# Kernel optimization log

Measured on AMD Instinct MI355X. Metric: run time of the kernel, lower is better.

The kernel has to match this reference:

```python
import jax, jax.numpy as jnp
import numpy as np

# ---- config matching init_kwargs ----
B, D, U = 8192, 1024, 512
F, E, T = 4, 4, 2
MAX_VAL = 10000000000.0
MIN_VAL = -10000000000.0
DISC_IDX = np.array([[0, 1, 2, 3], [4, 5, 6, 7]])  # discrete fields 0,1: per-expert feature index
CONT_IDX = np.array([8, 9])                         # continuous fields 2,3: single feature index
BOUNDS = np.array([-0.5, 0.0, 0.5])                 # 3 boundaries -> 4 buckets per continuous field
LOWERS = np.concatenate([[MIN_VAL], BOUNDS]).astype(np.float32)
UPPERS = np.concatenate([BOUNDS, [MAX_VAL]]).astype(np.float32)


def setup_inputs() -> dict:
    key = jax.random.key(0)
    ks = jax.random.split(key, 8)
    s_in = 1.0 / np.sqrt(D)
    s_cat = 1.0 / np.sqrt(2 * U)
    x = jax.random.normal(ks[0], (B, D), dtype=jnp.float32)
    Wc = jax.random.normal(ks[1], (D, U), dtype=jnp.float32) * s_in      # common expert kernel
    bc = jnp.zeros((U,), dtype=jnp.float32)
    We = jax.random.normal(ks[2], (F, E, D, U), dtype=jnp.float32) * s_in  # per-field per-expert kernels
    be = jnp.zeros((F, E, U), dtype=jnp.float32)
    Wg = jax.random.normal(ks[3], (T, D, F + 1), dtype=jnp.float32) * s_in  # per-task gate kernels
    bg = jnp.zeros((T, F + 1), dtype=jnp.float32)
    Wa = jax.random.normal(ks[4], (F, 2 * U, 1), dtype=jnp.float32) * s_cat  # attention kernels
    ba = jnp.zeros((F, 1), dtype=jnp.float32)
    Wu = jax.random.normal(ks[5], (F, 2 * U, 1), dtype=jnp.float32) * s_cat  # update kernels
    bu = jnp.zeros((F, 1), dtype=jnp.float32)
    return {"x": x, "Wc": Wc, "bc": bc, "We": We, "be": be,
            "Wg": Wg, "bg": bg, "Wa": Wa, "ba": ba, "Wu": Wu, "bu": bu}


def _field_masks(x):
    # discrete fields: expert j active iff x[:, idx[i][j]] > 0
    m_disc = x[:, DISC_IDX] > 0.0                         # [B, 2, E]
    # continuous fields: bucket x[:, idx] by boundaries (lower < v <= upper)
    v = x[:, CONT_IDX][..., None]                         # [B, 2, 1]
    m_cont = (v > LOWERS) & (v <= UPPERS)                 # [B, 2, E]
    return jnp.concatenate([m_disc, m_cont], axis=1).astype(x.dtype)  # [B, F, E]


def reference(x, Wc, bc, We, be, Wg, bg, Wa, ba, Wu, bu):
    # common expert: [B, U]
    common = jax.nn.relu(x @ Wc + bc)
    # all field experts at once: [B, F, E, U]
    e = jax.nn.relu(jnp.einsum('bd,fedu->bfeu', x, We) + be)
    mask = _field_masks(x)                                # [B, F, E]
    # mask-select active expert(s) per field: [B, F, U]
    field_out = jnp.einsum('bfe,bfeu->bfu', mask, e)
    # concat [common, field] per field: [B, F, 2U]
    cat = jnp.concatenate(
        [jnp.broadcast_to(common[:, None, :], field_out.shape), field_out], axis=-1)
    # sigmoid attention reweights field expert output
    att = jax.nn.sigmoid(jnp.einsum('bfk,fko->bfo', cat, Wa) + ba[None])   # [B, F, 1]
    field_att = att * field_out
    # sigmoid update gate blends field expert with common expert
    upd = jax.nn.sigmoid(jnp.einsum('bfk,fko->bfo', cat, Wu) + bu[None])   # [B, F, 1]
    field_final = upd * field_att + (1.0 - upd) * common[:, None, :]       # [B, F, U]
    # experts = [common] + per-field outputs: [B, F+1, U]
    experts = jnp.concatenate([common[:, None, :], field_final], axis=1)
    # per-task softmax gates over F+1 experts: [B, T, F+1]
    gates = jax.nn.softmax(jnp.einsum('bd,tdg->btg', x, Wg) + bg[None], axis=-1)
    # task outputs: [B, T, U]
    return jnp.einsum('btg,bgu->btu', gates, experts)
```

## Files before the change

kernel.cpp:

```cpp
#include <hip/hip_runtime.h>

typedef unsigned short ushort_t;

#define B_SZ 8192
#define D_SZ 1024
#define U_SZ 512
#define F_SZ 4
#define E_SZ 4
#define T_SZ 2

typedef __attribute__((ext_vector_type(8))) short bf16x8;
typedef __attribute__((ext_vector_type(4))) float f32x4;
typedef __attribute__((ext_vector_type(8))) unsigned short u16x8;

__device__ __forceinline__ unsigned short f2bf(float f) {
  union { float f; unsigned int u; } v; v.f = f;
  unsigned int r = v.u + 0x7FFFu + ((v.u >> 16) & 1u);
  return (unsigned short)(r >> 16);
}
__device__ __forceinline__ float bf2f(unsigned short h) {
  union { unsigned int u; float f; } v; v.u = ((unsigned int)h) << 16;
  return v.f;
}

__device__ __forceinline__ void gload_lds16(const void* g, void* l) {
  __builtin_amdgcn_global_load_lds(
      (const __attribute__((address_space(1))) unsigned int*)g,
      (__attribute__((address_space(3))) unsigned int*)l, 16, 0, 0);
}

__global__ __launch_bounds__(256) void conv_x(const float* __restrict__ x,
                                              ushort_t* __restrict__ xbf) {
  const size_t i = ((size_t)blockIdx.x * 256 + threadIdx.x) * 8;
  const float4 a = *(const float4*)(x + i);
  const float4 c = *(const float4*)(x + i + 4);
  u16x8 o;
  o[0] = f2bf(a.x); o[1] = f2bf(a.y); o[2] = f2bf(a.z); o[3] = f2bf(a.w);
  o[4] = f2bf(c.x); o[5] = f2bf(c.y); o[6] = f2bf(c.z); o[7] = f2bf(c.w);
  *(u16x8*)(xbf + i) = o;
}

__global__ __launch_bounds__(128) void pat_k(const float* __restrict__ x,
                                             unsigned int* __restrict__ pat,
                                             unsigned int* __restrict__ rowinfo,
                                             int* __restrict__ blockhist) {
  __shared__ int hist[64];
  const int t = threadIdx.x;
  if (t < 64) hist[t] = 0;
  __syncthreads();
  const int b = blockIdx.x * 128 + t;
  const float4 a = *(const float4*)(x + (size_t)b * D_SZ);
  const float4 c = *(const float4*)(x + (size_t)b * D_SZ + 4);
  const float v0 = x[(size_t)b * D_SZ + 8];
  const float v1 = x[(size_t)b * D_SZ + 9];
  int pp[4];
  pp[0] = (int)(a.x > 0.f) | ((int)(a.y > 0.f) << 1) |
          ((int)(a.z > 0.f) << 2) | ((int)(a.w > 0.f) << 3);
  pp[1] = (int)(c.x > 0.f) | ((int)(c.y > 0.f) << 1) |
          ((int)(c.z > 0.f) << 2) | ((int)(c.w > 0.f) << 3);
  const float LO[4] = {-1e10f, -0.5f, 0.f, 0.5f};
  const float HI[4] = {-0.5f, 0.f, 0.5f, 1e10f};
  pp[2] = 0; pp[3] = 0;
#pragma unroll
  for (int j = 0; j < 4; ++j) {
    if ((v0 > LO[j]) && (v0 <= HI[j])) pp[2] = 1 << j;
    if ((v1 > LO[j]) && (v1 <= HI[j])) pp[3] = 1 << j;
  }
  pat[b] = (unsigned int)(pp[0] | (pp[1] << 4) | (pp[2] << 8) | (pp[3] << 12));
  unsigned int info = 0;
#pragma unroll
  for (int f = 0; f < 4; ++f) {
    if (pp[f]) {
      const int lp = atomicAdd(&hist[f * 16 + pp[f]], 1);
      info |= (unsigned int)lp << (8 * f);
    }
  }
  rowinfo[b] = info;
  __syncthreads();
  if (t < 64) blockhist[blockIdx.x * 64 + t] = hist[t];
}

__global__ __launch_bounds__(64) void scan_k(const int* __restrict__ blockhist,
                                             int* __restrict__ base,
                                             int* __restrict__ cnt,
                                             int* __restrict__ dir,
                                             int* __restrict__ ntiles) {
  const int fp = threadIdx.x;
  int run = 0;
  for (int blk = 0; blk < 64; ++blk) {
    base[blk * 64 + fp] = run;
    run += blockhist[blk * 64 + fp];
  }
  cnt[fp] = run;
  __syncthreads();
  if (fp < 4) {
    const int f = fp;
    int idx = 0;
    for (int pop = 4; pop >= 1; --pop) {
      for (int p = 1; p < 16; ++p) {
        if (__popc(p) != pop) continue;
        const int n = cnt[f * 16 + p];
        const int nt = (n + 127) >> 7;
        for (int k = 0; k < nt; ++k) dir[f * 80 + idx++] = p | (k << 8);
      }
    }
    ntiles[f] = idx;
  }
}

__global__ __launch_bounds__(128) void scat_k(const unsigned int* __restrict__ pat,
                                              const unsigned int* __restrict__ rowinfo,
                                              const int* __restrict__ base,
                                              int* __restrict__ rowidx) {
  const int t = threadIdx.x;
  const int b = blockIdx.x * 128 + t;
  const unsigned int pv = pat[b];
  const unsigned int info = rowinfo[b];
#pragma unroll
  for (int f = 0; f < 4; ++f) {
    const int p = (int)((pv >> (4 * f)) & 15u);
    if (p) {
      const int pos = base[blockIdx.x * 64 + f * 16 + p] + (int)((info >> (8 * f)) & 255u);
      rowidx[((size_t)(f * 16 + p)) * B_SZ + pos] = b;
    }
  }
}

__global__ __launch_bounds__(256) void conv_w(const float* __restrict__ Wc,
                                              const float* __restrict__ We,
                                              ushort_t* __restrict__ wbf) {
  const int blk = blockIdx.x;
  const int midx = blk >> 7;
  const int tid = blk & 127;
  const int trow = (tid >> 3) * 64;
  const int tcol = (tid & 7) * 64;
  const float* src = (midx == 0) ? Wc : (We + (size_t)(midx - 1) * D_SZ * U_SZ);
  ushort_t* dst = wbf + (size_t)midx * U_SZ * D_SZ;

  __shared__ float tile[64][69];
  const int t = threadIdx.x;
  const int r0 = t >> 2;
  const int cseg = (t & 3) * 16;
#pragma unroll
  for (int j = 0; j < 4; ++j) {
    const float4 v = *(const float4*)(src + (size_t)(trow + r0) * U_SZ + tcol + cseg + j * 4);
    tile[r0][cseg + j * 4 + 0] = v.x;
    tile[r0][cseg + j * 4 + 1] = v.y;
    tile[r0][cseg + j * 4 + 2] = v.z;
    tile[r0][cseg + j * 4 + 3] = v.w;
  }
  __syncthreads();
  const int u = t >> 2;
  const int d0 = (t & 3) * 16;
#pragma unroll
  for (int h = 0; h < 2; ++h) {
    u16x8 ov;
#pragma unroll
    for (int k = 0; k < 8; ++k) ov[k] = f2bf(tile[d0 + h * 8 + k][u]);
    *(u16x8*)(dst + (size_t)(tcol + u) * D_SZ + trow + d0 + h * 8) = ov;
  }
}

__global__ __launch_bounds__(256) void gates_k(const float* __restrict__ x,
                                               const float* __restrict__ Wg,
                                               const float* __restrict__ bg,
                                               float* __restrict__ gates) {
  __shared__ float wgT[10 * 1024];
  const int t = threadIdx.x;
#pragma unroll
  for (int j = 0; j < 40; ++j) {
    const int i = j * 256 + t;
    const int t2 = i / 5120;
    const int rem = i - t2 * 5120;
    const int d = rem / 5;
    const int g = rem - d * 5;
    wgT[(t2 * 5 + g) * 1024 + d] = Wg[i];
  }
  __syncthreads();
  const int lane = t & 63;
  const int w = t >> 6;
#pragma unroll
  for (int rr = 0; rr < 2; ++rr) {
    const int b = blockIdx.x * 8 + w * 2 + rr;
    const float* xr = x + (size_t)b * D_SZ;
    float p[10];
#pragma unroll
    for (int j = 0; j < 10; ++j) p[j] = 0.f;
#pragma unroll
    for (int i = 0; i < 4; ++i) {
      const int d0 = i * 256 + lane * 4;
      const float4 xv = *(const float4*)(xr + d0);
#pragma unroll
      for (int g = 0; g < 10; ++g) {
        const float4 wv = *(const float4*)(wgT + g * 1024 + d0);
        p[g] += xv.x * wv.x + xv.y * wv.y + xv.z * wv.z + xv.w * wv.w;
      }
    }
#pragma unroll
    for (int off = 32; off > 0; off >>= 1)
#pragma unroll
      for (int j = 0; j < 10; ++j) p[j] += __shfl_xor(p[j], off);
    float l[10];
#pragma unroll
    for (int j = 0; j < 10; ++j) l[j] = p[j] + bg[j];
    const float mx0 = fmaxf(fmaxf(fmaxf(l[0], l[1]), fmaxf(l[2], l[3])), l[4]);
    const float mx1 = fmaxf(fmaxf(fmaxf(l[5], l[6]), fmaxf(l[7], l[8])), l[9]);
    float ev[10]; float s0 = 0.f, s1 = 0.f;
#pragma unroll
    for (int g = 0; g < 5; ++g) { ev[g] = expf(l[g] - mx0); s0 += ev[g]; }
#pragma unroll
    for (int g = 5; g < 10; ++g) { ev[g] = expf(l[g] - mx1); s1 += ev[g]; }
    if (lane < 5) gates[(size_t)b * 10 + lane] = ev[lane] / s0;
    else if (lane < 10) gates[(size_t)b * 10 + lane] = ev[lane] / s1;
  }
}

__global__ __launch_bounds__(256, 2) void gemm2(
    const ushort_t* __restrict__ xbf, const ushort_t* __restrict__ wbf,
    const int* __restrict__ rowidx, const int* __restrict__ cnt,
    const int* __restrict__ dir, const int* __restrict__ ntiles,
    const float* __restrict__ bc, const float* __restrict__ be,
    ushort_t* __restrict__ common, ushort_t* __restrict__ fout) {
  __shared__ ushort_t Ash[128 * 64];
  __shared__ ushort_t Bsh[128 * 64];
  __shared__ int ridx[128];

  const int t = threadIdx.x;
  const int lane = t & 63;
  const int w = t >> 6;
  const int wm = w >> 1;
  const int wn = w & 1;
  const int quad = lane >> 4;
  const int l16 = lane & 15;
  const int f = blockIdx.y;
  const int slot = blockIdx.x;
  const int u0 = blockIdx.z * 128;
  const bool isCommon = (f == 4);

  int p = 0, nrows = 128;
  if (isCommon) {
    if (slot >= 64) return;
    if (t < 128) ridx[t] = slot * 128 + t;
  } else {
    if (slot >= ntiles[f]) return;
    const int entry = dir[f * 80 + slot];
    p = entry & 15;
    const int tw = entry >> 8;
    const int n = cnt[f * 16 + p];
    const int rbase = tw * 128;
    nrows = min(128, n - rbase);
    if (t < 128) {
      const int rr = rbase + ((t < nrows) ? t : 0);
      ridx[t] = rowidx[((size_t)f * 16 + p) * B_SZ + rr];
    }
  }
  __syncthreads();

  size_t aoff[4]; int boff[4]; int ldsoff[4];
#pragma unroll
  for (int i = 0; i < 4; ++i) {
    const int c = (w * 4 + i) * 64 + lane;
    const int r = c >> 3;
    const int gc = (c & 7) ^ (r & 7);
    aoff[i] = (size_t)ridx[r] * D_SZ + gc * 8;
    boff[i] = r * D_SZ + gc * 8;
    ldsoff[i] = (w * 4 + i) * 1024;
  }

  int rowA[4], rowB[4];
#pragma unroll
  for (int i = 0; i < 4; ++i) {
    rowA[i] = wm * 64 + i * 16 + l16;
    rowB[i] = wn * 64 + i * 16 + l16;
  }
  int sw[2];
  sw[0] = ((quad) ^ (l16 & 7)) * 8;
  sw[1] = ((4 + quad) ^ (l16 & 7)) * 8;

  int elist[4]; int ne = 0;
  if (isCommon) { elist[0] = 0; ne = 1; }
  else {
#pragma unroll
    for (int e = 0; e < 4; ++e)
      if (p & (1 << e)) elist[ne++] = e;
  }

  const f32x4 fzero = {0.f, 0.f, 0.f, 0.f};
  f32x4 facc[4][4];
#pragma unroll
  for (int mi = 0; mi < 4; ++mi)
#pragma unroll
    for (int ni = 0; ni < 4; ++ni) facc[mi][ni] = fzero;

  for (int ei = 0; ei < ne; ++ei) {
    const int midx = isCommon ? 0 : (1 + f * 4 + elist[ei]);
    const ushort_t* wbase = wbf + (size_t)midx * (U_SZ * D_SZ) + (size_t)u0 * D_SZ;
    f32x4 acc[4][4];
#pragma unroll
    for (int mi = 0; mi < 4; ++mi)
#pragma unroll
      for (int ni = 0; ni < 4; ++ni) acc[mi][ni] = fzero;

    for (int k0 = 0; k0 < D_SZ; k0 += 64) {
#pragma unroll
      for (int i = 0; i < 4; ++i) {
        gload_lds16(xbf + aoff[i] + k0, (char*)Ash + ldsoff[i]);
        gload_lds16(wbase + boff[i] + k0, (char*)Bsh + ldsoff[i]);
      }
      __syncthreads();
#pragma unroll
      for (int qs = 0; qs < 2; ++qs) {
        bf16x8 av[4], bv[4];
#pragma unroll
        for (int mi = 0; mi < 4; ++mi)
          av[mi] = *(const bf16x8*)(Ash + rowA[mi] * 64 + sw[qs]);
#pragma unroll
        for (int ni = 0; ni < 4; ++ni)
          bv[ni] = *(const bf16x8*)(Bsh + rowB[ni] * 64 + sw[qs]);
#pragma unroll
        for (int mi = 0; mi < 4; ++mi)
#pragma unroll
          for (int ni = 0; ni < 4; ++ni)
            acc[mi][ni] = __builtin_amdgcn_mfma_f32_16x16x32_bf16(av[mi], bv[ni],
                                                                  acc[mi][ni], 0, 0, 0);
      }
      __syncthreads();
    }

    if (isCommon) {
#pragma unroll
      for (int mi = 0; mi < 4; ++mi) {
        const int rowb = slot * 128 + wm * 64 + mi * 16 + quad * 4;
#pragma unroll
        for (int ni = 0; ni < 4; ++ni) {
          const int u = u0 + wn * 64 + ni * 16 + l16;
          const float bcv = bc[u];
#pragma unroll
          for (int r = 0; r < 4; ++r) {
            const float v = fmaxf(acc[mi][ni][r] + bcv, 0.f);
            common[(size_t)(rowb + r) * U_SZ + u] = f2bf(v);
          }
        }
      }
    } else {
      const float* bevp = be + (size_t)(f * 4 + elist[ei]) * U_SZ;
#pragma unroll
      for (int ni = 0; ni < 4; ++ni) {
        const int u = u0 + wn * 64 + ni * 16 + l16;
        const float bev = bevp[u];
#pragma unroll
        for (int mi = 0; mi < 4; ++mi)
#pragma unroll
          for (int r = 0; r < 4; ++r)
            facc[mi][ni][r] += fmaxf(acc[mi][ni][r] + bev, 0.f);
      }
    }
  }

  if (!isCommon) {
#pragma unroll
    for (int mi = 0; mi < 4; ++mi) {
      const int rowl = wm * 64 + mi * 16 + quad * 4;
#pragma unroll
      for (int r = 0; r < 4; ++r) {
        if (rowl + r < nrows) {
          const int brow = ridx[rowl + r];
#pragma unroll
          for (int ni = 0; ni < 4; ++ni) {
            const int u = u0 + wn * 64 + ni * 16 + l16;
            fout[((size_t)brow * F_SZ + f) * U_SZ + u] = f2bf(facc[mi][ni][r]);
          }
        }
      }
    }
  }
}

__global__ __launch_bounds__(256) void stage2_k(
    const ushort_t* __restrict__ common, const ushort_t* __restrict__ fout,
    const unsigned int* __restrict__ pat, const float* __restrict__ gates,
    const float* __restrict__ Wa, const float* __restrict__ ba,
    const float* __restrict__ Wu, const float* __restrict__ bu,
    float* __restrict__ out) {
  const int b = blockIdx.x;
  const int t = threadIdx.x;
  const int lane = t & 63;
  const int w = t >> 6;
  const unsigned int pv = pat[b];

  const float c0 = bf2f(common[(size_t)b * U_SZ + t]);
  const float c1 = bf2f(common[(size_t)b * U_SZ + 256 + t]);
  float fo0[4], fo1[4];
#pragma unroll
  for (int f = 0; f < 4; ++f) {
    const bool act = ((pv >> (4 * f)) & 15u) != 0u;
    fo0[f] = act ? bf2f(fout[((size_t)b * F_SZ + f) * U_SZ + t]) : 0.f;
    fo1[f] = act ? bf2f(fout[((size_t)b * F_SZ + f) * U_SZ + 256 + t]) : 0.f;
  }
  float pa[4], pu[4];
#pragma unroll
  for (int f = 0; f < 4; ++f) {
    const float* wa = Wa + f * 1024;
    pa[f] = c0 * wa[t] + c1 * wa[256 + t] + fo0[f] * wa[512 + t] + fo1[f] * wa[768 + t];
    const float* wu = Wu + f * 1024;
    pu[f] = c0 * wu[t] + c1 * wu[256 + t] + fo0[f] * wu[512 + t] + fo1[f] * wu[768 + t];
  }
#pragma unroll
  for (int off = 32; off > 0; off >>= 1) {
#pragma unroll
    for (int f = 0; f < 4; ++f) {
      pa[f] += __shfl_xor(pa[f], off);
      pu[f] += __shfl_xor(pu[f], off);
    }
  }
  __shared__ float redA[4][4];
  __shared__ float redU[4][4];
  __shared__ float gsh[10];
  if (lane == 0) {
#pragma unroll
    for (int f = 0; f < 4; ++f) { redA[w][f] = pa[f]; redU[w][f] = pu[f]; }
  }
  if (t < 10) gsh[t] = gates[(size_t)b * 10 + t];
  __syncthreads();
  float ff0[4], ff1[4];
#pragma unroll
  for (int f = 0; f < 4; ++f) {
    const float sa = redA[0][f] + redA[1][f] + redA[2][f] + redA[3][f] + ba[f];
    const float su = redU[0][f] + redU[1][f] + redU[2][f] + redU[3][f] + bu[f];
    const float att = 1.f / (1.f + expf(-sa));
    const float upd = 1.f / (1.f + expf(-su));
    ff0[f] = upd * (att * fo0[f]) + (1.f - upd) * c0;
    ff1[f] = upd * (att * fo1[f]) + (1.f - upd) * c1;
  }
#pragma unroll
  for (int t2 = 0; t2 < 2; ++t2) {
    float v0 = gsh[t2 * 5] * c0;
    float v1 = gsh[t2 * 5] * c1;
#pragma unroll
    for (int f = 0; f < 4; ++f) {
      v0 += gsh[t2 * 5 + 1 + f] * ff0[f];
      v1 += gsh[t2 * 5 + 1 + f] * ff1[f];
    }
    out[((size_t)b * T_SZ + t2) * U_SZ + t] = v0;
    out[((size_t)b * T_SZ + t2) * U_SZ + 256 + t] = v1;
  }
}

extern "C" void kernel_launch(void* const* d_in, const int* in_sizes, int n_in,
                              void* d_out, int out_size, void* d_ws, size_t ws_size,
                              hipStream_t stream) {
  (void)in_sizes; (void)n_in; (void)out_size; (void)ws_size;
  const float* x  = (const float*)d_in[0];
  const float* Wc = (const float*)d_in[1];
  const float* bc = (const float*)d_in[2];
  const float* We = (const float*)d_in[3];
  const float* be = (const float*)d_in[4];
  const float* Wg = (const float*)d_in[5];
  const float* bg = (const float*)d_in[6];
  const float* Wa = (const float*)d_in[7];
  const float* ba = (const float*)d_in[8];
  const float* Wu = (const float*)d_in[9];
  const float* bu = (const float*)d_in[10];
  float* out = (float*)d_out;
  char* ws = (char*)d_ws;

  const size_t O_XBF    = 0;
  const size_t O_WBF    = O_XBF + (size_t)B_SZ * D_SZ * 2;
  const size_t O_PAT    = O_WBF + (size_t)17 * U_SZ * D_SZ * 2;
  const size_t O_ROWIDX = O_PAT + (size_t)B_SZ * 4;
  const size_t O_CNT    = O_ROWIDX + (size_t)4 * 16 * B_SZ * 4;
  const size_t O_DIR    = O_CNT + 256;
  const size_t O_NT     = O_DIR + 1280;
  const size_t O_GATES  = O_NT + 16;
  const size_t O_COMMON = O_GATES + (size_t)B_SZ * 10 * 4;
  const size_t O_FOUT   = O_COMMON + (size_t)B_SZ * U_SZ * 2;
  const size_t O_RINFO  = O_FOUT + (size_t)B_SZ * F_SZ * U_SZ * 2;
  const size_t O_BHIST  = O_RINFO + (size_t)B_SZ * 4;
  const size_t O_BASE   = O_BHIST + 64 * 64 * 4;

  ushort_t* xbf     = (ushort_t*)(ws + O_XBF);
  ushort_t* wbf     = (ushort_t*)(ws + O_WBF);
  unsigned int* patp= (unsigned int*)(ws + O_PAT);
  int*      rowidxp = (int*)(ws + O_ROWIDX);
  int*      cntp    = (int*)(ws + O_CNT);
  int*      dirp    = (int*)(ws + O_DIR);
  int*      ntp     = (int*)(ws + O_NT);
  float*    gatesp  = (float*)(ws + O_GATES);
  ushort_t* commonp = (ushort_t*)(ws + O_COMMON);
  ushort_t* foutp   = (ushort_t*)(ws + O_FOUT);
  unsigned int* rinfop = (unsigned int*)(ws + O_RINFO);
  int*      bhistp  = (int*)(ws + O_BHIST);
  int*      basep   = (int*)(ws + O_BASE);

  conv_x<<<dim3(4096), dim3(256), 0, stream>>>(x, xbf);
  pat_k<<<dim3(64), dim3(128), 0, stream>>>(x, patp, rinfop, bhistp);
  scan_k<<<dim3(1), dim3(64), 0, stream>>>(bhistp, basep, cntp, dirp, ntp);
  scat_k<<<dim3(64), dim3(128), 0, stream>>>(patp, rinfop, basep, rowidxp);
  conv_w<<<dim3(17 * 128), dim3(256), 0, stream>>>(Wc, We, wbf);
  gates_k<<<dim3(1024), dim3(256), 0, stream>>>(x, Wg, bg, gatesp);
  gemm2<<<dim3(80, 5, 4), dim3(256), 0, stream>>>(xbf, wbf, rowidxp, cntp, dirp, ntp,
                                                  bc, be, commonp, foutp);
  stage2_k<<<dim3(8192), dim3(256), 0, stream>>>(commonp, foutp, patp, gatesp,
                                                 Wa, ba, Wu, bu, out);
}
```

Before: 331.3 us.

## Merge prep kernels into one launch and widen GEMM tile to 256 columns

Folds the x conversion, weight transpose-conversion, gate softmax and pattern histogram kernels into a single prep kernel dispatched by block index, and merges scan and scatter into one 1024-thread block. This cuts launch count and the small serial kernels between stages. The grouped GEMM now uses 512-thread blocks covering 256 output columns, so each A tile loaded from gathered rows is reused across twice as many columns, at the cost of more LDS per block. The scan/scatter stage now runs in one block, which serialises that work.

```diff
diff --git a/kernel.cpp b/kernel.cpp
--- a/kernel.cpp
+++ b/kernel.cpp
@@ -29,212 +29,208 @@
       (__attribute__((address_space(3))) unsigned int*)l, 16, 0, 0);
 }
 
-__global__ __launch_bounds__(256) void conv_x(const float* __restrict__ x,
-                                              ushort_t* __restrict__ xbf) {
-  const size_t i = ((size_t)blockIdx.x * 256 + threadIdx.x) * 8;
-  const float4 a = *(const float4*)(x + i);
-  const float4 c = *(const float4*)(x + i + 4);
-  u16x8 o;
-  o[0] = f2bf(a.x); o[1] = f2bf(a.y); o[2] = f2bf(a.z); o[3] = f2bf(a.w);
-  o[4] = f2bf(c.x); o[5] = f2bf(c.y); o[6] = f2bf(c.z); o[7] = f2bf(c.w);
-  *(u16x8*)(xbf + i) = o;
-}
-
-__global__ __launch_bounds__(128) void pat_k(const float* __restrict__ x,
-                                             unsigned int* __restrict__ pat,
-                                             unsigned int* __restrict__ rowinfo,
-                                             int* __restrict__ blockhist) {
-  __shared__ int hist[64];
+__global__ __launch_bounds__(256) void prep_k(
+    const float* __restrict__ x, const float* __restrict__ Wc,
+    const float* __restrict__ We, const float* __restrict__ Wg,
+    const float* __restrict__ bg,
+    ushort_t* __restrict__ xbf, ushort_t* __restrict__ wbf,
+    float* __restrict__ gates, unsigned int* __restrict__ pat,
+    unsigned int* __restrict__ rowinfo, int* __restrict__ blockhist) {
+  __shared__ __align__(16) char smem[40960];
+  const int bid = blockIdx.x;
   const int t = threadIdx.x;
-  if (t < 64) hist[t] = 0;
+
+  if (bid < 4096) {
+    const size_t i = ((size_t)bid * 256 + t) * 8;
+    const float4 a = *(const float4*)(x + i);
+    const float4 c = *(const float4*)(x + i + 4);
+    u16x8 o;
+    o[0] = f2bf(a.x); o[1] = f2bf(a.y); o[2] = f2bf(a.z); o[3] = f2bf(a.w);
+    o[4] = f2bf(c.x); o[5] = f2bf(c.y); o[6] = f2bf(c.z); o[7] = f2bf(c.w);
+    *(u16x8*)(xbf + i) = o;
+  } else if (bid < 6272) {
+    const int blk = bid - 4096;
+    const int midx = blk >> 7;
+    const int tid = blk & 127;
+    const int trow = (tid >> 3) * 64;
+    const int tcol = (tid & 7) * 64;
+    const float* src = (midx == 0) ? Wc : (We + (size_t)(midx - 1) * D_SZ * U_SZ);
+    ushort_t* dst = wbf + (size_t)midx * U_SZ * D_SZ;
+    float (*tile)[69] = (float(*)[69])smem;
+    const int r0 = t >> 2;
+    const int cseg = (t & 3) * 16;
+#pragma unroll
+    for (int j = 0; j < 4; ++j) {
+      const float4 v = *(const float4*)(src + (size_t)(trow + r0) * U_SZ + tcol + cseg + j * 4);
+      tile[r0][cseg + j * 4 + 0] = v.x;
+      tile[r0][cseg + j * 4 + 1] = v.y;
+      tile[r0][cseg + j * 4 + 2] = v.z;
+      tile[r0][cseg + j * 4 + 3] = v.w;
+    }
+    __syncthreads();
+    const int u = t >> 2;
+    const int d0 = (t & 3) * 16;
+#pragma unroll
+    for (int h = 0; h < 2; ++h) {
+      u16x8 ov;
+#pragma unroll
+      for (int k = 0; k < 8; ++k) ov[k] = f2bf(tile[d0 + h * 8 + k][u]);
+      *(u16x8*)(dst + (size_t)(tcol + u) * D_SZ + trow + d0 + h * 8) = ov;
+    }
+  } else if (bid < 7296) {
+    const int gb = bid - 6272;
+    float* wgT = (float*)smem;
+#pragma unroll
+    for (int j = 0; j < 40; ++j) {
+      const int i = j * 256 + t;
+      const int t2 = i / 5120;
+      const int rem = i - t2 * 5120;
+      const int d = rem / 5;
+      const int g = rem - d * 5;
+      wgT[(t2 * 5 + g) * 1024 + d] = Wg[i];
+    }
+    __syncthreads();
+    const int lane = t & 63;
+    const int w = t >> 6;
+#pragma unroll
+    for (int rr = 0; rr < 2; ++rr) {
+      const int b = gb * 8 + w * 2 + rr;
+      const float* xr = x + (size_t)b * D_SZ;
+      float p[10];
+#pragma unroll
+      for (int j = 0; j < 10; ++j) p[j] = 0.f;
+#pragma unroll
+      for (int i = 0; i < 4; ++i) {
+        const int d0 = i * 256 + lane * 4;
+        const float4 xv = *(const float4*)(xr + d0);
+#pragma unroll
+        for (int g = 0; g < 10; ++g) {
+          const float4 wv = *(const float4*)(wgT + g * 1024 + d0);
+          p[g] += xv.x * wv.x + xv.y * wv.y + xv.z * wv.z + xv.w * wv.w;
+        }
+      }
+#pragma unroll
+      for (int off = 32; off > 0; off >>= 1)
+#pragma unroll
+        for (int j = 0; j < 10; ++j) p[j] += __shfl_xor(p[j], off);
+      float l[10];
+#pragma unroll
+      for (int j = 0; j < 10; ++j) l[j] = p[j] + bg[j];
+      const float mx0 = fmaxf(fmaxf(fmaxf(l[0], l[1]), fmaxf(l[2], l[3])), l[4]);
+      const float mx1 = fmaxf(fmaxf(fmaxf(l[5], l[6]), fmaxf(l[7], l[8])), l[9]);
+      float ev[10]; float s0 = 0.f, s1 = 0.f;
+#pragma unroll
+      for (int g = 0; g < 5; ++g) { ev[g] = expf(l[g] - mx0); s0 += ev[g]; }
+#pragma unroll
+      for (int g = 5; g < 10; ++g) { ev[g] = expf(l[g] - mx1); s1 += ev[g]; }
+      if (lane < 5) gates[(size_t)b * 10 + lane] = ev[lane] / s0;
+      else if (lane < 10) gates[(size_t)b * 10 + lane] = ev[lane] / s1;
+    }
+  } else {
+    const int pb = bid - 7296;
+    int* hist = (int*)smem;
+    if (t < 64) hist[t] = 0;
+    __syncthreads();
+    const int b = pb * 256 + t;
+    const float4 a = *(const float4*)(x + (size_t)b * D_SZ);
+    const float4 c = *(const float4*)(x + (size_t)b * D_SZ + 4);
+    const float v0 = x[(size_t)b * D_SZ + 8];
+    const float v1 = x[(size_t)b * D_SZ + 9];
+    int pp[4];
+    pp[0] = (int)(a.x > 0.f) | ((int)(a.y > 0.f) << 1) |
+            ((int)(a.z > 0.f) << 2) | ((int)(a.w > 0.f) << 3);
+    pp[1] = (int)(c.x > 0.f) | ((int)(c.y > 0.f) << 1) |
+            ((int)(c.z > 0.f) << 2) | ((int)(c.w > 0.f) << 3);
+    const float LO[4] = {-1e10f, -0.5f, 0.f, 0.5f};
+    const float HI[4] = {-0.5f, 0.f, 0.5f, 1e10f};
+    pp[2] = 0; pp[3] = 0;
+#pragma unroll
+    for (int j = 0; j < 4; ++j) {
+      if ((v0 > LO[j]) && (v0 <= HI[j])) pp[2] = 1 << j;
+      if ((v1 > LO[j]) && (v1 <= HI[j])) pp[3] = 1 << j;
+    }
+    pat[b] = (unsigned int)(pp[0] | (pp[1] << 4) | (pp[2] << 8) | (pp[3] << 12));
+    unsigned int info = 0;
+#pragma unroll
+    for (int f = 0; f < 4; ++f) {
+      if (pp[f]) {
+        const int lp = atomicAdd(&hist[f * 16 + pp[f]], 1);
+        info |= (unsigned int)lp << (8 * f);
+      }
+    }
+    rowinfo[b] = info;
+    __syncthreads();
+    if (t < 64) blockhist[pb * 64 + t] = hist[t];
+  }
+}
+
+__global__ __launch_bounds__(1024) void scanscat_k(
+    const int* __restrict__ blockhist, const unsigned int* __restrict__ pat,
+    const unsigned int* __restrict__ rowinfo,
+    int* __restrict__ rowidx, int* __restrict__ cnt,
+    int* __restrict__ dir, int* __restrict__ ntiles) {
+  __shared__ int sbase[32 * 64];
+  const int t = threadIdx.x;
+  if (t < 64) {
+    int run = 0;
+    for (int blk = 0; blk < 32; ++blk) {
+      sbase[blk * 64 + t] = run;
+      run += blockhist[blk * 64 + t];
+    }
+    cnt[t] = run;
+  }
   __syncthreads();
-  const int b = blockIdx.x * 128 + t;
-  const float4 a = *(const float4*)(x + (size_t)b * D_SZ);
-  const float4 c = *(const float4*)(x + (size_t)b * D_SZ + 4);
-  const float v0 = x[(size_t)b * D_SZ + 8];
-  const float v1 = x[(size_t)b * D_SZ + 9];
-  int pp[4];
-  pp[0] = (int)(a.x > 0.f) | ((int)(a.y > 0.f) << 1) |
-          ((int)(a.z > 0.f) << 2) | ((int)(a.w > 0.f) << 3);
-  pp[1] = (int)(c.x > 0.f) | ((int)(c.y > 0.f) << 1) |
-          ((int)(c.z > 0.f) << 2) | ((int)(c.w > 0.f) << 3);
-  const float LO[4] = {-1e10f, -0.5f, 0.f, 0.5f};
-  const float HI[4] = {-0.5f, 0.f, 0.5f, 1e10f};
-  pp[2] = 0; pp[3] = 0;
-#pragma unroll
-  for (int j = 0; j < 4; ++j) {
-    if ((v0 > LO[j]) && (v0 <= HI[j])) pp[2] = 1 << j;
-    if ((v1 > LO[j]) && (v1 <= HI[j])) pp[3] = 1 << j;
-  }
-  pat[b] = (unsigned int)(pp[0] | (pp[1] << 4) | (pp[2] << 8) | (pp[3] << 12));
-  unsigned int info = 0;
-#pragma unroll
-  for (int f = 0; f < 4; ++f) {
-    if (pp[f]) {
-      const int lp = atomicAdd(&hist[f * 16 + pp[f]], 1);
-      info |= (unsigned int)lp << (8 * f);
-    }
-  }
-  rowinfo[b] = info;
-  __syncthreads();
-  if (t < 64) blockhist[blockIdx.x * 64 + t] = hist[t];
-}
-
-__global__ __launch_bounds__(64) void scan_k(const int* __restrict__ blockhist,
-                                             int* __restrict__ base,
-                                             int* __restrict__ cnt,
-                                             int* __restrict__ dir,
-                                             int* __restrict__ ntiles) {
-  const int fp = threadIdx.x;
-  int run = 0;
-  for (int blk = 0; blk < 64; ++blk) {
-    base[blk * 64 + fp] = run;
-    run += blockhist[blk * 64 + fp];
-  }
-  cnt[fp] = run;
-  __syncthreads();
-  if (fp < 4) {
-    const int f = fp;
+  if (t < 4) {
+    const int f = t;
     int idx = 0;
     for (int pop = 4; pop >= 1; --pop) {
       for (int p = 1; p < 16; ++p) {
         if (__popc(p) != pop) continue;
-        const int n = cnt[f * 16 + p];
+        int n = 0;
+        for (int blk = 0; blk < 32; ++blk) n += blockhist[blk * 64 + f * 16 + p];
         const int nt = (n + 127) >> 7;
         for (int k = 0; k < nt; ++k) dir[f * 80 + idx++] = p | (k << 8);
       }
     }
     ntiles[f] = idx;
   }
-}
-
-__global__ __launch_bounds__(128) void scat_k(const unsigned int* __restrict__ pat,
-                                              const unsigned int* __restrict__ rowinfo,
-                                              const int* __restrict__ base,
-                                              int* __restrict__ rowidx) {
-  const int t = threadIdx.x;
-  const int b = blockIdx.x * 128 + t;
-  const unsigned int pv = pat[b];
-  const unsigned int info = rowinfo[b];
-#pragma unroll
-  for (int f = 0; f < 4; ++f) {
-    const int p = (int)((pv >> (4 * f)) & 15u);
-    if (p) {
-      const int pos = base[blockIdx.x * 64 + f * 16 + p] + (int)((info >> (8 * f)) & 255u);
-      rowidx[((size_t)(f * 16 + p)) * B_SZ + pos] = b;
-    }
-  }
-}
-
-__global__ __launch_bounds__(256) void conv_w(const float* __restrict__ Wc,
-                                              const float* __restrict__ We,
-                                              ushort_t* __restrict__ wbf) {
-  const int blk = blockIdx.x;
-  const int midx = blk >> 7;
-  const int tid = blk & 127;
-  const int trow = (tid >> 3) * 64;
-  const int tcol = (tid & 7) * 64;
-  const float* src = (midx == 0) ? Wc : (We + (size_t)(midx - 1) * D_SZ * U_SZ);
-  ushort_t* dst = wbf + (size_t)midx * U_SZ * D_SZ;
-
-  __shared__ float tile[64][69];
-  const int t = threadIdx.x;
-  const int r0 = t >> 2;
-  const int cseg = (t & 3) * 16;
-#pragma unroll
-  for (int j = 0; j < 4; ++j) {
-    const float4 v = *(const float4*)(src + (size_t)(trow + r0) * U_SZ + tcol + cseg + j * 4);
-    tile[r0][cseg + j * 4 + 0] = v.x;
-    tile[r0][cseg + j * 4 + 1] = v.y;
-    tile[r0][cseg + j * 4 + 2] = v.z;
-    tile[r0][cseg + j * 4 + 3] = v.w;
-  }
-  __syncthreads();
-  const int u = t >> 2;
-  const int d0 = (t & 3) * 16;
-#pragma unroll
-  for (int h = 0; h < 2; ++h) {
-    u16x8 ov;
-#pragma unroll
-    for (int k = 0; k < 8; ++k) ov[k] = f2bf(tile[d0 + h * 8 + k][u]);
-    *(u16x8*)(dst + (size_t)(tcol + u) * D_SZ + trow + d0 + h * 8) = ov;
-  }
-}
-
-__global__ __launch_bounds__(256) void gates_k(const float* __restrict__ x,
-                                               const float* __restrict__ Wg,
-                                               const float* __restrict__ bg,
-                                               float* __restrict__ gates) {
-  __shared__ float wgT[10 * 1024];
-  const int t = threadIdx.x;
-#pragma unroll
-  for (int j = 0; j < 40; ++j) {
-    const int i = j * 256 + t;
-    const int t2 = i / 5120;
-    const int rem = i - t2 * 5120;
-    const int d = rem / 5;
-    const int g = rem - d * 5;
-    wgT[(t2 * 5 + g) * 1024 + d] = Wg[i];
-  }
-  __syncthreads();
-  const int lane = t & 63;
-  const int w = t >> 6;
-#pragma unroll
-  for (int rr = 0; rr < 2; ++rr) {
-    const int b = blockIdx.x * 8 + w * 2 + rr;
-    const float* xr = x + (size_t)b * D_SZ;
-    float p[10];
-#pragma unroll
-    for (int j = 0; j < 10; ++j) p[j] = 0.f;
-#pragma unroll
-    for (int i = 0; i < 4; ++i) {
-      const int d0 = i * 256 + lane * 4;
-      const float4 xv = *(const float4*)(xr + d0);
-#pragma unroll
-      for (int g = 0; g < 10; ++g) {
-        const float4 wv = *(const float4*)(wgT + g * 1024 + d0);
-        p[g] += xv.x * wv.x + xv.y * wv.y + xv.z * wv.z + xv.w * wv.w;
-      }
-    }
-#pragma unroll
-    for (int off = 32; off > 0; off >>= 1)
-#pragma unroll
-      for (int j = 0; j < 10; ++j) p[j] += __shfl_xor(p[j], off);
-    float l[10];
-#pragma unroll
-    for (int j = 0; j < 10; ++j) l[j] = p[j] + bg[j];
-    const float mx0 = fmaxf(fmaxf(fmaxf(l[0], l[1]), fmaxf(l[2], l[3])), l[4]);
-    const float mx1 = fmaxf(fmaxf(fmaxf(l[5], l[6]), fmaxf(l[7], l[8])), l[9]);
-    float ev[10]; float s0 = 0.f, s1 = 0.f;
-#pragma unroll
-    for (int g = 0; g < 5; ++g) { ev[g] = expf(l[g] - mx0); s0 += ev[g]; }
-#pragma unroll
-    for (int g = 5; g < 10; ++g) { ev[g] = expf(l[g] - mx1); s1 += ev[g]; }
-    if (lane < 5) gates[(size_t)b * 10 + lane] = ev[lane] / s0;
-    else if (lane < 10) gates[(size_t)b * 10 + lane] = ev[lane] / s1;
-  }
-}
-
-__global__ __launch_bounds__(256, 2) void gemm2(
+#pragma unroll
+  for (int it = 0; it < 8; ++it) {
+    const int b = it * 1024 + t;
+    const unsigned int pv = pat[b];
+    const unsigned int info = rowinfo[b];
+    const int blk = b >> 8;
+#pragma unroll
+    for (int f = 0; f < 4; ++f) {
+      const int p = (int)((pv >> (4 * f)) & 15u);
+      if (p) {
+        const int pos = sbase[blk * 64 + f * 16 + p] + (int)((info >> (8 * f)) & 255u);
+        rowidx[((size_t)(f * 16 + p)) * B_SZ + pos] = b;
+      }
+    }
+  }
+}
+
+__global__ __launch_bounds__(512, 4) void gemm2(
     const ushort_t* __restrict__ xbf, const ushort_t* __restrict__ wbf,
     const int* __restrict__ rowidx, const int* __restrict__ cnt,
     const int* __restrict__ dir, const int* __restrict__ ntiles,
     const float* __restrict__ bc, const float* __restrict__ be,
     ushort_t* __restrict__ common, ushort_t* __restrict__ fout) {
   __shared__ ushort_t Ash[128 * 64];
-  __shared__ ushort_t Bsh[128 * 64];
+  __shared__ ushort_t Bsh[256 * 64];
   __shared__ int ridx[128];
 
   const int t = threadIdx.x;
   const int lane = t & 63;
   const int w = t >> 6;
-  const int wm = w >> 1;
-  const int wn = w & 1;
+  const int wm = w >> 2;
+  const int wn = w & 3;
   const int quad = lane >> 4;
   const int l16 = lane & 15;
   const int f = blockIdx.y;
   const int slot = blockIdx.x;
-  const int u0 = blockIdx.z * 128;
+  const int u0 = blockIdx.z * 256;
   const bool isCommon = (f == 4);
 
   int p = 0, nrows = 128;
@@ -256,15 +252,23 @@
   }
   __syncthreads();
 
-  size_t aoff[4]; int boff[4]; int ldsoff[4];
+  size_t aoff[2]; int aldsoff[2];
+#pragma unroll
+  for (int i = 0; i < 2; ++i) {
+    const int c = (w * 2 + i) * 64 + lane;
+    const int r = c >> 3;
+    const int gc = (c & 7) ^ (r & 7);
+    aoff[i] = (size_t)ridx[r] * D_SZ + gc * 8;
+    aldsoff[i] = (w * 2 + i) * 1024;
+  }
+  int boff[4]; int bldsoff[4];
 #pragma unroll
   for (int i = 0; i < 4; ++i) {
     const int c = (w * 4 + i) * 64 + lane;
     const int r = c >> 3;
     const int gc = (c & 7) ^ (r & 7);
-    aoff[i] = (size_t)ridx[r] * D_SZ + gc * 8;
     boff[i] = r * D_SZ + gc * 8;
-    ldsoff[i] = (w * 4 + i) * 1024;
+    bldsoff[i] = (w * 4 + i) * 1024;
   }
 
   int rowA[4], rowB[4];
@@ -303,10 +307,11 @@
 
     for (int k0 = 0; k0 < D_SZ; k0 += 64) {
 #pragma unroll
-      for (int i = 0; i < 4; ++i) {
-        gload_lds16(xbf + aoff[i] + k0, (char*)Ash + ldsoff[i]);
-        gload_lds16(wbase + boff[i] + k0, (char*)Bsh + ldsoff[i]);
-      }
+      for (int i = 0; i < 2; ++i)
+        gload_lds16(xbf + aoff[i] + k0, (char*)Ash + aldsoff[i]);
+#pragma unroll
+      for (int i = 0; i < 4; ++i)
+        gload_lds16(wbase + boff[i] + k0, (char*)Bsh + bldsoff[i]);
       __syncthreads();
 #pragma unroll
       for (int qs = 0; qs < 2; ++qs) {
@@ -476,7 +481,6 @@
   const size_t O_FOUT   = O_COMMON + (size_t)B_SZ * U_SZ * 2;
   const size_t O_RINFO  = O_FOUT + (size_t)B_SZ * F_SZ * U_SZ * 2;
   const size_t O_BHIST  = O_RINFO + (size_t)B_SZ * 4;
-  const size_t O_BASE   = O_BHIST + 64 * 64 * 4;
 
   ushort_t* xbf     = (ushort_t*)(ws + O_XBF);
   ushort_t* wbf     = (ushort_t*)(ws + O_WBF);
@@ -490,15 +494,12 @@
   ushort_t* foutp   = (ushort_t*)(ws + O_FOUT);
   unsigned int* rinfop = (unsigned int*)(ws + O_RINFO);
   int*      bhistp  = (int*)(ws + O_BHIST);
-  int*      basep   = (int*)(ws + O_BASE);
-
-  conv_x<<<dim3(4096), dim3(256), 0, stream>>>(x, xbf);
-  pat_k<<<dim3(64), dim3(128), 0, stream>>>(x, patp, rinfop, bhistp);
-  scan_k<<<dim3(1), dim3(64), 0, stream>>>(bhistp, basep, cntp, dirp, ntp);
-  scat_k<<<dim3(64), dim3(128), 0, stream>>>(patp, rinfop, basep, rowidxp);
-  conv_w<<<dim3(17 * 128), dim3(256), 0, stream>>>(Wc, We, wbf);
-  gates_k<<<dim3(1024), dim3(256), 0, stream>>>(x, Wg, bg, gatesp);
-  gemm2<<<dim3(80, 5, 4), dim3(256), 0, stream>>>(xbf, wbf, rowidxp, cntp, dirp, ntp,
+
+  prep_k<<<dim3(7328), dim3(256), 0, stream>>>(x, Wc, We, Wg, bg, xbf, wbf,
+                                               gatesp, patp, rinfop, bhistp);
+  scanscat_k<<<dim3(1), dim3(1024), 0, stream>>>(bhistp, patp, rinfop,
+                                                 rowidxp, cntp, dirp, ntp);
+  gemm2<<<dim3(80, 5, 2), dim3(512), 0, stream>>>(xbf, wbf, rowidxp, cntp, dirp, ntp,
                                                   bc, be, commonp, foutp);
   stage2_k<<<dim3(8192), dim3(256), 0, stream>>>(commonp, foutp, patp, gatesp,
                                                  Wa, ba, Wu, bu, out);
```

Result: slower. 470.7 us (+42.1%).
